# Kernel tuning notes

Hardware: AMD Instinct MI355X
Metric: run time of the kernel (lower is better)

## Reference

```python
import math
import jax, jax.numpy as jnp
import numpy as np

B, S, D, H = 4, 2048, 1024, 16
DH = D // H  # 64


def setup_inputs() -> dict:
    key = jax.random.key(0)
    k1, k2, k3 = jax.random.split(key, 3)
    x = jax.random.normal(k1, (B, S, D), dtype=jnp.float32)
    W_qkv = jax.random.normal(k2, (D, 3 * D), dtype=jnp.float32) * (1.0 / math.sqrt(D))
    b_qkv = jax.random.normal(k3, (3 * D,), dtype=jnp.float32) * 0.02
    return {"x": x, "W_qkv": W_qkv, "b_qkv": b_qkv}


def reference(x, W_qkv, b_qkv):
    b, s, d = x.shape
    qkv = x @ W_qkv + b_qkv                       # [B,S,3D]
    # Faithful to torch: view(B,S,H,3,D_h) -> interleaved per-head q/k/v split
    qkv = qkv.reshape(b, s, H, 3, DH)
    q = jnp.transpose(qkv[:, :, :, 0, :], (0, 2, 1, 3))  # [B,H,S,DH]
    k = jnp.transpose(qkv[:, :, :, 1, :], (0, 2, 1, 3))
    v = jnp.transpose(qkv[:, :, :, 2, :], (0, 2, 1, 3))
    scores = jnp.einsum('bhsd,bhtd->bhst', q, k) / math.sqrt(DH)  # [B,H,S,S]
    causal = jnp.triu(jnp.ones((s, s), dtype=bool), k=1)
    scores = jnp.where(causal, -jnp.inf, scores)
    weights = jax.nn.softmax(scores, axis=-1)
    # dropout is identity in eval/reference mode
    context = jnp.einsum('bhst,bhtd->bhsd', weights, v)  # [B,H,S,DH]
    return jnp.transpose(context, (0, 2, 1, 3)).reshape(b, s, d)
```

## Files before the change

kernel.cpp:

```cpp
#include <hip/hip_runtime.h>
#include <hip/hip_bf16.h>

#define Bz 4
#define Sz 2048
#define Dz 1024
#define Hz 16
#define DHz 64
#define Mz (Bz*Sz)
#define N3z (3*Dz)
#define Kz Dz

typedef short s16x8 __attribute__((ext_vector_type(8)));
typedef float f32x4 __attribute__((ext_vector_type(4)));
typedef unsigned short u16;

__device__ __forceinline__ u16 f2b(float f) {
  union { float f; unsigned u; } v; v.f = f;
  unsigned r = v.u + 0x7FFFu + ((v.u >> 16) & 1u);
  return (u16)(r >> 16);
}

__device__ __forceinline__ unsigned cvt_pk_bf16(float lo, float hi) {
  unsigned r;
  asm("v_cvt_pk_bf16_f32 %0, %1, %2" : "=v"(r) : "v"(lo), "v"(hi));
  return r;
}

__global__ __launch_bounds__(256) void cvt_x(const float* __restrict__ x,
                                             u16* __restrict__ xb) {
  int i = (blockIdx.x * 256 + threadIdx.x) * 4;
  float4 v = *reinterpret_cast<const float4*>(x + i);
  ushort4 o;
  o.x = f2b(v.x); o.y = f2b(v.y); o.z = f2b(v.z); o.w = f2b(v.w);
  *reinterpret_cast<ushort4*>(xb + i) = o;
}

__global__ __launch_bounds__(256) void transpose_w(const float* __restrict__ W,
                                                   u16* __restrict__ Wt) {
  __shared__ u16 t[32][33];
  int nb = blockIdx.x;
  int kb = blockIdx.y;
  int tx = threadIdx.x, ty = threadIdx.y;
#pragma unroll
  for (int j = 0; j < 4; ++j) {
    int k = kb * 32 + ty + j * 8;
    t[ty + j * 8][tx] = f2b(W[(size_t)k * N3z + nb * 32 + tx]);
  }
  __syncthreads();
#pragma unroll
  for (int j = 0; j < 4; ++j) {
    int n = nb * 32 + ty + j * 8;
    Wt[(size_t)n * Kz + kb * 32 + tx] = t[tx][ty + j * 8];
  }
}

#define BM 128
#define BN 128
#define BKs 64
#define QSCALE (0.125f * 1.44269504088896f)

__global__ __launch_bounds__(256) void qkv_gemm(
    const u16* __restrict__ A, const u16* __restrict__ Bt,
    const float* __restrict__ bias,
    u16* __restrict__ Qo, u16* __restrict__ Ko, u16* __restrict__ Vo) {
  __shared__ alignas(16) u16 As[BM * BKs];
  __shared__ alignas(16) u16 Bs[BN * BKs];
  const int tid = threadIdx.x;
  const int wid = tid >> 6, lane = tid & 63;
  const int wr = wid >> 1, wc = wid & 1;
  const int g = lane >> 4, lq = lane & 15;
  const int brow = blockIdx.x * BM;
  const int bcol = blockIdx.y * BN;

  const int soff = (((lane & 7) ^ (lane >> 3))) * 8;

  f32x4 acc[4][4] = {};

  for (int kt = 0; kt < Kz; kt += BKs) {
#pragma unroll
    for (int c = 0; c < 4; ++c) {
      int row = (wid * 4 + c) * 8 + (lane >> 3);
      const u16* ga = A + (size_t)(brow + row) * Kz + kt + soff;
      __builtin_amdgcn_global_load_lds(
          (const __attribute__((address_space(1))) void*)ga,
          (__attribute__((address_space(3))) void*)&As[(wid * 4 + c) * 512],
          16, 0, 0);
      const u16* gb = Bt + (size_t)(bcol + row) * Kz + kt + soff;
      __builtin_amdgcn_global_load_lds(
          (const __attribute__((address_space(1))) void*)gb,
          (__attribute__((address_space(3))) void*)&Bs[(wid * 4 + c) * 512],
          16, 0, 0);
    }
    __syncthreads();

#pragma unroll
    for (int ks = 0; ks < 2; ++ks) {
      s16x8 af[4], bfr[4];
#pragma unroll
      for (int i = 0; i < 4; ++i) {
        int rowa = wr * 64 + i * 16 + lq;
        int rowb = wc * 64 + i * 16 + lq;
        int sl = ((ks * 4 + g) ^ (lq & 7)) << 4;
        af[i]  = *reinterpret_cast<const s16x8*>((const char*)As + rowa * 128 + sl);
        bfr[i] = *reinterpret_cast<const s16x8*>((const char*)Bs + rowb * 128 + sl);
      }
#pragma unroll
      for (int mi = 0; mi < 4; ++mi)
#pragma unroll
        for (int ni = 0; ni < 4; ++ni)
          acc[mi][ni] = __builtin_amdgcn_mfma_f32_16x16x32_bf16(af[mi], bfr[ni], acc[mi][ni], 0, 0, 0);
    }
    __syncthreads();
  }

#pragma unroll
  for (int ni = 0; ni < 4; ++ni) {
    int gcol = bcol + wc * 64 + ni * 16 + lq;
    int h = gcol / 192;
    int rem = gcol - h * 192;
    int tt = rem >> 6;
    int dh = rem & 63;
    float bv = bias[gcol];
    u16* dst = (tt == 0) ? Qo : (tt == 1) ? Ko : Vo;
    float scale = (tt == 0) ? QSCALE : 1.0f;
#pragma unroll
    for (int mi = 0; mi < 4; ++mi) {
#pragma unroll
      for (int r = 0; r < 4; ++r) {
        int grow = brow + wr * 64 + mi * 16 + g * 4 + r;
        int bb = grow >> 11;
        int ss = grow & 2047;
        float v = (acc[mi][ni][r] + bv) * scale;
        dst[(((size_t)bb * Hz + h) * Sz + ss) * DHz + dh] = f2b(v);
      }
    }
  }
}

__global__ __launch_bounds__(512, 4) void attn_kernel(
    const u16* __restrict__ Qg, const u16* __restrict__ Kg,
    const u16* __restrict__ Vg, float* __restrict__ out) {
  __shared__ alignas(16) u16 Ks[2][64 * 64];
  __shared__ alignas(16) u16 Vs[2][64 * 64];

  const int qpair = blockIdx.x;
  const int bh = blockIdx.y;
  const int tid = threadIdx.x;
  const int wid = tid >> 6, lane = tid & 63;
  const int g = lane >> 4, lq = lane & 15;
  const size_t base = (size_t)bh * Sz * DHz;
  const int b = bh >> 4, h = bh & 15;

  const int krow = tid >> 3;
  const int kslot = tid & 7;
  const int kswz = kslot ^ (krow & 7);
  const int vkey = tid & 63;
  const int vdh0 = (tid >> 6) * 8;

  const int p = g & 1;
  const int cb = g >> 1;
  const int sA = 32 * (g & 1) + lq;
  const int sB = sA + 16;
  const int sEven = cb ? sB : sA;
  const int sOdd  = cb ? sA : sB;

  for (int half = 0; half < 2; ++half) {
    const int qt = half ? (15 - qpair) : qpair;
    const int q0w = qt * 128 + wid * 16;
    const int qrow = q0w + lq;

    s16x8 qf0 = *reinterpret_cast<const s16x8*>(Qg + base + (size_t)(q0w + lq) * DHz + g * 8);
    s16x8 qf1 = *reinterpret_cast<const s16x8*>(Qg + base + (size_t)(q0w + lq) * DHz + g * 8 + 32);

    f32x4 o[4] = {};
    float m1 = -1e30f;
    float l1 = 0.f;

    const int nt = 2 * qt + 2;

    {
      s16x8 kc = *reinterpret_cast<const s16x8*>(Kg + base + (size_t)krow * DHz + kslot * 8);
      s16x8 vc = *reinterpret_cast<const s16x8*>(Vg + base + (size_t)vkey * DHz + vdh0);
      char* KB = (char*)Ks[0];
      char* VB = (char*)Vs[0];
      *reinterpret_cast<s16x8*>(KB + krow * 128 + kswz * 16) = kc;
#pragma unroll
      for (int j = 0; j < 8; ++j)
        *reinterpret_cast<u16*>(VB + (((vdh0 + j) * 128 + vkey * 2) ^ (j << 4))) = (u16)vc[j];
    }
    __syncthreads();

    int cur = 0;
    for (int t = 0; t < nt; ++t) {
      const int kv0 = t * 64;
      const bool more = (t + 1 < nt);

      s16x8 kn, vn;
      if (more) {
        const int nv0 = kv0 + 64;
        kn = *reinterpret_cast<const s16x8*>(Kg + base + (size_t)(nv0 + krow) * DHz + kslot * 8);
        vn = *reinterpret_cast<const s16x8*>(Vg + base + (size_t)(nv0 + vkey) * DHz + vdh0);
      }

      const char* KsC = (const char*)Ks[0] + cur * 8192;
      const char* VsC = (const char*)Vs[0] + cur * 8192;

      const bool active = (kv0 <= q0w + 15);
      if (active) {
        f32x4 z[4];
#pragma unroll
        for (int f = 0; f < 4; ++f) {
          int row = f * 16 + lq;
          s16x8 kb0 = *reinterpret_cast<const s16x8*>(KsC + row * 128 + ((g ^ (row & 7)) << 4));
          s16x8 kb1 = *reinterpret_cast<const s16x8*>(KsC + row * 128 + (((g + 4) ^ (row & 7)) << 4));
          f32x4 zz = {0.f, 0.f, 0.f, 0.f};
          zz = __builtin_amdgcn_mfma_f32_16x16x32_bf16(kb0, qf0, zz, 0, 0, 0);
          zz = __builtin_amdgcn_mfma_f32_16x16x32_bf16(kb1, qf1, zz, 0, 0, 0);
          z[f] = zz;
        }

        if (kv0 + 63 > q0w) {
#pragma unroll
          for (int f = 0; f < 4; ++f)
#pragma unroll
            for (int r = 0; r < 4; ++r) {
              int key = kv0 + f * 16 + g * 4 + r;
              if (key > qrow) z[f][r] = -1e30f;
            }
        }

        float pm = z[0][0];
#pragma unroll
        for (int f = 0; f < 4; ++f)
#pragma unroll
          for (int r = 0; r < 4; ++r) pm = fmaxf(pm, z[f][r]);
        pm = fmaxf(pm, __shfl_xor(pm, 16));
        pm = fmaxf(pm, __shfl_xor(pm, 32));

        if (!__all(pm <= m1 + 8.0f)) {
          float mn = fmaxf(m1, pm);
          float a = exp2f(m1 - mn);
          m1 = mn;
          l1 *= a;
          float a0 = __shfl(a, 4 * g + 0);
          float a1 = __shfl(a, 4 * g + 1);
          float a2 = __shfl(a, 4 * g + 2);
          float a3 = __shfl(a, 4 * g + 3);
#pragma unroll
          for (int ni = 0; ni < 4; ++ni) {
            o[ni][0] *= a0; o[ni][1] *= a1; o[ni][2] *= a2; o[ni][3] *= a3;
          }
        }

        float s = 0.f;
        unsigned w[4][2];
#pragma unroll
        for (int f = 0; f < 4; ++f) {
          float p0 = exp2f(z[f][0] - m1);
          float p1 = exp2f(z[f][1] - m1);
          float p2 = exp2f(z[f][2] - m1);
          float p3 = exp2f(z[f][3] - m1);
          s += (p0 + p1) + (p2 + p3);
          w[f][0] = cvt_pk_bf16(p0, p1);
          w[f][1] = cvt_pk_bf16(p2, p3);
        }
        s += __shfl_xor(s, 16);
        s += __shfl_xor(s, 32);
        l1 += s;

        int e0 = __shfl((int)(p ? w[1][0] : w[0][0]), sEven);
        int o0 = __shfl((int)(p ? w[0][0] : w[1][0]), sOdd);
        int e1 = __shfl((int)(p ? w[1][1] : w[0][1]), sEven);
        int o1 = __shfl((int)(p ? w[0][1] : w[1][1]), sOdd);
        int e2 = __shfl((int)(p ? w[3][0] : w[2][0]), sEven);
        int o2 = __shfl((int)(p ? w[2][0] : w[3][0]), sOdd);
        int e3 = __shfl((int)(p ? w[3][1] : w[2][1]), sEven);
        int o3 = __shfl((int)(p ? w[2][1] : w[3][1]), sOdd);
        union { int i[4]; s16x8 v; } A0, A1;
        A0.i[0] = cb ? o0 : e0;
        A0.i[2] = cb ? e0 : o0;
        A0.i[1] = cb ? o1 : e1;
        A0.i[3] = cb ? e1 : o1;
        A1.i[0] = cb ? o2 : e2;
        A1.i[2] = cb ? e2 : o2;
        A1.i[1] = cb ? o3 : e3;
        A1.i[3] = cb ? e3 : o3;

#pragma unroll
        for (int ni = 0; ni < 4; ++ni) {
          int row = ni * 16 + lq;
          s16x8 vb0 = *reinterpret_cast<const s16x8*>(VsC + row * 128 + ((g ^ (row & 7)) << 4));
          s16x8 vb1 = *reinterpret_cast<const s16x8*>(VsC + row * 128 + (((g + 4) ^ (row & 7)) << 4));
          o[ni] = __builtin_amdgcn_mfma_f32_16x16x32_bf16(A0.v, vb0, o[ni], 0, 0, 0);
          o[ni] = __builtin_amdgcn_mfma_f32_16x16x32_bf16(A1.v, vb1, o[ni], 0, 0, 0);
        }
      }

      if (more) {
        char* KB = (char*)Ks[0] + (cur ^ 1) * 8192;
        char* VB = (char*)Vs[0] + (cur ^ 1) * 8192;
        *reinterpret_cast<s16x8*>(KB + krow * 128 + kswz * 16) = kn;
#pragma unroll
        for (int j = 0; j < 8; ++j)
          *reinterpret_cast<u16*>(VB + (((vdh0 + j) * 128 + vkey * 2) ^ (j << 4))) = (u16)vn[j];
      }
      __syncthreads();
      cur ^= 1;
    }

    float lr0 = __shfl(l1, 4 * g + 0);
    float lr1 = __shfl(l1, 4 * g + 1);
    float lr2 = __shfl(l1, 4 * g + 2);
    float lr3 = __shfl(l1, 4 * g + 3);
    float inv[4] = {1.0f / lr0, 1.0f / lr1, 1.0f / lr2, 1.0f / lr3};
#pragma unroll
    for (int r = 0; r < 4; ++r) {
      int s = q0w + g * 4 + r;
      float* op = out + (((size_t)b * Sz + s) * Hz + h) * DHz;
#pragma unroll
      for (int ni = 0; ni < 4; ++ni)
        op[ni * 16 + lq] = o[ni][r] * inv[r];
    }
  }
}

extern "C" void kernel_launch(void* const* d_in, const int* in_sizes, int n_in,
                              void* d_out, int out_size, void* d_ws, size_t ws_size,
                              hipStream_t stream) {
  const float* x    = (const float*)d_in[0];
  const float* W    = (const float*)d_in[1];
  const float* bias = (const float*)d_in[2];
  float* out = (float*)d_out;

  char* ws = (char*)d_ws;
  u16* xb = (u16*)(ws);
  u16* wt = (u16*)(ws + 16777216);
  u16* Qb = (u16*)(ws + 23068672);
  u16* Kb = (u16*)(ws + 39845888);
  u16* Vb = (u16*)(ws + 56623104);

  cvt_x<<<8192, 256, 0, stream>>>(x, xb);
  transpose_w<<<dim3(96, 32), dim3(32, 8), 0, stream>>>(W, wt);
  qkv_gemm<<<dim3(Mz / BM, N3z / BN), 256, 0, stream>>>(xb, wt, bias, Qb, Kb, Vb);
  attn_kernel<<<dim3(8, Bz * Hz), 512, 0, stream>>>(Qb, Kb, Vb, out);
}
```

Before: 238.5 us.

## Store V transposed, load K/V via global_load_lds, fuse paired query tiles

The QKV GEMM now writes V in a transposed [B,H,DH,S] layout. This lets the attention kernel stream both K and V tiles straight into LDS with global_load_lds, replacing the register round-trip and 8 scattered 16-bit LDS stores per V tile. The two query tiles of each block (qp and 15-qp) are now processed in one pass over K/V, so shared keys are loaded once and the tile synchronisation is shared. Block indices in both kernels are remapped for XCD/L2 locality. The GEMM epilogue now does strided V stores and the attention kernel holds two accumulators sets, which raises register pressure.

```diff
diff --git a/kernel.cpp b/kernel.cpp
--- a/kernel.cpp
+++ b/kernel.cpp
@@ -62,15 +62,20 @@
 __global__ __launch_bounds__(256) void qkv_gemm(
     const u16* __restrict__ A, const u16* __restrict__ Bt,
     const float* __restrict__ bias,
-    u16* __restrict__ Qo, u16* __restrict__ Ko, u16* __restrict__ Vo) {
+    u16* __restrict__ Qo, u16* __restrict__ Ko, u16* __restrict__ Vt) {
   __shared__ alignas(16) u16 As[BM * BKs];
   __shared__ alignas(16) u16 Bs[BN * BKs];
   const int tid = threadIdx.x;
   const int wid = tid >> 6, lane = tid & 63;
   const int wr = wid >> 1, wc = wid & 1;
   const int g = lane >> 4, lq = lane & 15;
-  const int brow = blockIdx.x * BM;
-  const int bcol = blockIdx.y * BN;
+
+  const int id = blockIdx.x + gridDim.x * blockIdx.y;
+  const int xc = id & 7, rr = id >> 3;
+  const int bx = xc * 8 + (rr & 7);
+  const int by = rr >> 3;
+  const int brow = bx * BM;
+  const int bcol = by * BN;
 
   const int soff = (((lane & 7) ^ (lane >> 3))) * 8;
 
@@ -121,8 +126,9 @@
     int tt = rem >> 6;
     int dh = rem & 63;
     float bv = bias[gcol];
-    u16* dst = (tt == 0) ? Qo : (tt == 1) ? Ko : Vo;
+    u16* dst = (tt == 0) ? Qo : (tt == 1) ? Ko : Vt;
     float scale = (tt == 0) ? QSCALE : 1.0f;
+    bool isv = (tt == 2);
 #pragma unroll
     for (int mi = 0; mi < 4; ++mi) {
 #pragma unroll
@@ -131,31 +137,130 @@
         int bb = grow >> 11;
         int ss = grow & 2047;
         float v = (acc[mi][ni][r] + bv) * scale;
-        dst[(((size_t)bb * Hz + h) * Sz + ss) * DHz + dh] = f2b(v);
+        size_t off = isv ? ((((size_t)bb * Hz + h) * DHz + dh) * Sz + ss)
+                         : ((((size_t)bb * Hz + h) * Sz + ss) * DHz + dh);
+        dst[off] = f2b(v);
       }
     }
+  }
+}
+
+__device__ __forceinline__ void attn_tile(
+    const char* KsC, const char* VsC, int kv0, int q0w, int qrow,
+    int g, int lq, int p, int cb, int sEven, int sOdd,
+    const s16x8& qf0, const s16x8& qf1,
+    f32x4 (&o)[4], float& m1, float& l1) {
+  if (kv0 > q0w + 15) return;
+
+  f32x4 z[4];
+#pragma unroll
+  for (int f = 0; f < 4; ++f) {
+    int row = f * 16 + lq;
+    s16x8 kb0 = *reinterpret_cast<const s16x8*>(KsC + row * 128 + ((g ^ (row & 7)) << 4));
+    s16x8 kb1 = *reinterpret_cast<const s16x8*>(KsC + row * 128 + (((g + 4) ^ (row & 7)) << 4));
+    f32x4 zz = {0.f, 0.f, 0.f, 0.f};
+    zz = __builtin_amdgcn_mfma_f32_16x16x32_bf16(kb0, qf0, zz, 0, 0, 0);
+    zz = __builtin_amdgcn_mfma_f32_16x16x32_bf16(kb1, qf1, zz, 0, 0, 0);
+    z[f] = zz;
+  }
+
+  if (kv0 + 63 > q0w) {
+#pragma unroll
+    for (int f = 0; f < 4; ++f)
+#pragma unroll
+      for (int r = 0; r < 4; ++r) {
+        int key = kv0 + f * 16 + g * 4 + r;
+        if (key > qrow) z[f][r] = -1e30f;
+      }
+  }
+
+  float pm = z[0][0];
+#pragma unroll
+  for (int f = 0; f < 4; ++f)
+#pragma unroll
+    for (int r = 0; r < 4; ++r) pm = fmaxf(pm, z[f][r]);
+  pm = fmaxf(pm, __shfl_xor(pm, 16));
+  pm = fmaxf(pm, __shfl_xor(pm, 32));
+
+  if (!__all(pm <= m1 + 8.0f)) {
+    float mn = fmaxf(m1, pm);
+    float a = exp2f(m1 - mn);
+    m1 = mn;
+    l1 *= a;
+    float a0 = __shfl(a, 4 * g + 0);
+    float a1 = __shfl(a, 4 * g + 1);
+    float a2 = __shfl(a, 4 * g + 2);
+    float a3 = __shfl(a, 4 * g + 3);
+#pragma unroll
+    for (int ni = 0; ni < 4; ++ni) {
+      o[ni][0] *= a0; o[ni][1] *= a1; o[ni][2] *= a2; o[ni][3] *= a3;
+    }
+  }
+
+  float s = 0.f;
+  unsigned w[4][2];
+#pragma unroll
+  for (int f = 0; f < 4; ++f) {
+    float p0 = exp2f(z[f][0] - m1);
+    float p1 = exp2f(z[f][1] - m1);
+    float p2 = exp2f(z[f][2] - m1);
+    float p3 = exp2f(z[f][3] - m1);
+    s += (p0 + p1) + (p2 + p3);
+    w[f][0] = cvt_pk_bf16(p0, p1);
+    w[f][1] = cvt_pk_bf16(p2, p3);
+  }
+  s += __shfl_xor(s, 16);
+  s += __shfl_xor(s, 32);
+  l1 += s;
+
+  int e0 = __shfl((int)(p ? w[1][0] : w[0][0]), sEven);
+  int o0 = __shfl((int)(p ? w[0][0] : w[1][0]), sOdd);
+  int e1 = __shfl((int)(p ? w[1][1] : w[0][1]), sEven);
+  int o1 = __shfl((int)(p ? w[0][1] : w[1][1]), sOdd);
+  int e2 = __shfl((int)(p ? w[3][0] : w[2][0]), sEven);
+  int o2 = __shfl((int)(p ? w[2][0] : w[3][0]), sOdd);
+  int e3 = __shfl((int)(p ? w[3][1] : w[2][1]), sEven);
+  int o3 = __shfl((int)(p ? w[2][1] : w[3][1]), sOdd);
+  union { int i[4]; s16x8 v; } A0, A1;
+  A0.i[0] = cb ? o0 : e0;
+  A0.i[2] = cb ? e0 : o0;
+  A0.i[1] = cb ? o1 : e1;
+  A0.i[3] = cb ? e1 : o1;
+  A1.i[0] = cb ? o2 : e2;
+  A1.i[2] = cb ? e2 : o2;
+  A1.i[1] = cb ? o3 : e3;
+  A1.i[3] = cb ? e3 : o3;
+
+#pragma unroll
+  for (int ni = 0; ni < 4; ++ni) {
+    int row = ni * 16 + lq;
+    s16x8 vb0 = *reinterpret_cast<const s16x8*>(VsC + row * 128 + ((g ^ (row & 7)) << 4));
+    s16x8 vb1 = *reinterpret_cast<const s16x8*>(VsC + row * 128 + (((g + 4) ^ (row & 7)) << 4));
+    o[ni] = __builtin_amdgcn_mfma_f32_16x16x32_bf16(A0.v, vb0, o[ni], 0, 0, 0);
+    o[ni] = __builtin_amdgcn_mfma_f32_16x16x32_bf16(A1.v, vb1, o[ni], 0, 0, 0);
   }
 }
 
 __global__ __launch_bounds__(512, 4) void attn_kernel(
     const u16* __restrict__ Qg, const u16* __restrict__ Kg,
-    const u16* __restrict__ Vg, float* __restrict__ out) {
+    const u16* __restrict__ Vtg, float* __restrict__ out) {
   __shared__ alignas(16) u16 Ks[2][64 * 64];
   __shared__ alignas(16) u16 Vs[2][64 * 64];
 
-  const int qpair = blockIdx.x;
-  const int bh = blockIdx.y;
   const int tid = threadIdx.x;
   const int wid = tid >> 6, lane = tid & 63;
   const int g = lane >> 4, lq = lane & 15;
+
+  const int id = blockIdx.x + 8 * blockIdx.y;
+  const int xc = id & 7, rr = id >> 3;
+  const int bh = xc * 8 + (rr & 7);
+  const int qp = rr >> 3;
+
   const size_t base = (size_t)bh * Sz * DHz;
   const int b = bh >> 4, h = bh & 15;
 
   const int krow = tid >> 3;
-  const int kslot = tid & 7;
-  const int kswz = kslot ^ (krow & 7);
-  const int vkey = tid & 63;
-  const int vdh0 = (tid >> 6) * 8;
+  const int sswz = ((tid & 7) ^ (krow & 7)) * 8;
 
   const int p = g & 1;
   const int cb = g >> 1;
@@ -164,150 +269,66 @@
   const int sEven = cb ? sB : sA;
   const int sOdd  = cb ? sA : sB;
 
+  const int qtA = qp, qtB = 15 - qp;
+  const int q0wA = qtA * 128 + wid * 16;
+  const int q0wB = qtB * 128 + wid * 16;
+  const int qrowA = q0wA + lq, qrowB = q0wB + lq;
+  const int ntA = 2 * qtA + 2, ntB = 2 * qtB + 2;
+
+  s16x8 qfA0 = *reinterpret_cast<const s16x8*>(Qg + base + (size_t)qrowA * DHz + g * 8);
+  s16x8 qfA1 = *reinterpret_cast<const s16x8*>(Qg + base + (size_t)qrowA * DHz + g * 8 + 32);
+  s16x8 qfB0 = *reinterpret_cast<const s16x8*>(Qg + base + (size_t)qrowB * DHz + g * 8);
+  s16x8 qfB1 = *reinterpret_cast<const s16x8*>(Qg + base + (size_t)qrowB * DHz + g * 8 + 32);
+
+  f32x4 oA[4] = {}, oB[4] = {};
+  float mA = -1e30f, lA = 0.f, mB = -1e30f, lB = 0.f;
+
+  {
+    const u16* gk = Kg + base + (size_t)krow * DHz + sswz;
+    __builtin_amdgcn_global_load_lds(
+        (const __attribute__((address_space(1))) void*)gk,
+        (__attribute__((address_space(3))) void*)&Ks[0][wid * 512], 16, 0, 0);
+    const u16* gv = Vtg + base + (size_t)krow * Sz + sswz;
+    __builtin_amdgcn_global_load_lds(
+        (const __attribute__((address_space(1))) void*)gv,
+        (__attribute__((address_space(3))) void*)&Vs[0][wid * 512], 16, 0, 0);
+  }
+  __syncthreads();
+
+  int cur = 0;
+  for (int t = 0; t < ntB; ++t) {
+    const int kv0 = t * 64;
+
+    if (t + 1 < ntB) {
+      const int nv0 = kv0 + 64;
+      const u16* gk = Kg + base + (size_t)(nv0 + krow) * DHz + sswz;
+      __builtin_amdgcn_global_load_lds(
+          (const __attribute__((address_space(1))) void*)gk,
+          (__attribute__((address_space(3))) void*)&Ks[cur ^ 1][wid * 512], 16, 0, 0);
+      const u16* gv = Vtg + base + (size_t)krow * Sz + nv0 + sswz;
+      __builtin_amdgcn_global_load_lds(
+          (const __attribute__((address_space(1))) void*)gv,
+          (__attribute__((address_space(3))) void*)&Vs[cur ^ 1][wid * 512], 16, 0, 0);
+    }
+
+    const char* KsC = (const char*)Ks[cur];
+    const char* VsC = (const char*)Vs[cur];
+
+    attn_tile(KsC, VsC, kv0, q0wB, qrowB, g, lq, p, cb, sEven, sOdd,
+              qfB0, qfB1, oB, mB, lB);
+    if (t < ntA)
+      attn_tile(KsC, VsC, kv0, q0wA, qrowA, g, lq, p, cb, sEven, sOdd,
+                qfA0, qfA1, oA, mA, lA);
+
+    __syncthreads();
+    cur ^= 1;
+  }
+
+#pragma unroll
   for (int half = 0; half < 2; ++half) {
-    const int qt = half ? (15 - qpair) : qpair;
-    const int q0w = qt * 128 + wid * 16;
-    const int qrow = q0w + lq;
-
-    s16x8 qf0 = *reinterpret_cast<const s16x8*>(Qg + base + (size_t)(q0w + lq) * DHz + g * 8);
-    s16x8 qf1 = *reinterpret_cast<const s16x8*>(Qg + base + (size_t)(q0w + lq) * DHz + g * 8 + 32);
-
-    f32x4 o[4] = {};
-    float m1 = -1e30f;
-    float l1 = 0.f;
-
-    const int nt = 2 * qt + 2;
-
-    {
-      s16x8 kc = *reinterpret_cast<const s16x8*>(Kg + base + (size_t)krow * DHz + kslot * 8);
-      s16x8 vc = *reinterpret_cast<const s16x8*>(Vg + base + (size_t)vkey * DHz + vdh0);
-      char* KB = (char*)Ks[0];
-      char* VB = (char*)Vs[0];
-      *reinterpret_cast<s16x8*>(KB + krow * 128 + kswz * 16) = kc;
-#pragma unroll
-      for (int j = 0; j < 8; ++j)
-        *reinterpret_cast<u16*>(VB + (((vdh0 + j) * 128 + vkey * 2) ^ (j << 4))) = (u16)vc[j];
-    }
-    __syncthreads();
-
-    int cur = 0;
-    for (int t = 0; t < nt; ++t) {
-      const int kv0 = t * 64;
-      const bool more = (t + 1 < nt);
-
-      s16x8 kn, vn;
-      if (more) {
-        const int nv0 = kv0 + 64;
-        kn = *reinterpret_cast<const s16x8*>(Kg + base + (size_t)(nv0 + krow) * DHz + kslot * 8);
-        vn = *reinterpret_cast<const s16x8*>(Vg + base + (size_t)(nv0 + vkey) * DHz + vdh0);
-      }
-
-      const char* KsC = (const char*)Ks[0] + cur * 8192;
-      const char* VsC = (const char*)Vs[0] + cur * 8192;
-
-      const bool active = (kv0 <= q0w + 15);
-      if (active) {
-        f32x4 z[4];
-#pragma unroll
-        for (int f = 0; f < 4; ++f) {
-          int row = f * 16 + lq;
-          s16x8 kb0 = *reinterpret_cast<const s16x8*>(KsC + row * 128 + ((g ^ (row & 7)) << 4));
-          s16x8 kb1 = *reinterpret_cast<const s16x8*>(KsC + row * 128 + (((g + 4) ^ (row & 7)) << 4));
-          f32x4 zz = {0.f, 0.f, 0.f, 0.f};
-          zz = __builtin_amdgcn_mfma_f32_16x16x32_bf16(kb0, qf0, zz, 0, 0, 0);
-          zz = __builtin_amdgcn_mfma_f32_16x16x32_bf16(kb1, qf1, zz, 0, 0, 0);
-          z[f] = zz;
-        }
-
-        if (kv0 + 63 > q0w) {
-#pragma unroll
-          for (int f = 0; f < 4; ++f)
-#pragma unroll
-            for (int r = 0; r < 4; ++r) {
-              int key = kv0 + f * 16 + g * 4 + r;
-              if (key > qrow) z[f][r] = -1e30f;
-            }
-        }
-
-        float pm = z[0][0];
-#pragma unroll
-        for (int f = 0; f < 4; ++f)
-#pragma unroll
-          for (int r = 0; r < 4; ++r) pm = fmaxf(pm, z[f][r]);
-        pm = fmaxf(pm, __shfl_xor(pm, 16));
-        pm = fmaxf(pm, __shfl_xor(pm, 32));
-
-        if (!__all(pm <= m1 + 8.0f)) {
-          float mn = fmaxf(m1, pm);
-          float a = exp2f(m1 - mn);
-          m1 = mn;
-          l1 *= a;
-          float a0 = __shfl(a, 4 * g + 0);
-          float a1 = __shfl(a, 4 * g + 1);
-          float a2 = __shfl(a, 4 * g + 2);
-          float a3 = __shfl(a, 4 * g + 3);
-#pragma unroll
-          for (int ni = 0; ni < 4; ++ni) {
-            o[ni][0] *= a0; o[ni][1] *= a1; o[ni][2] *= a2; o[ni][3] *= a3;
-          }
-        }
-
-        float s = 0.f;
-        unsigned w[4][2];
-#pragma unroll
-        for (int f = 0; f < 4; ++f) {
-          float p0 = exp2f(z[f][0] - m1);
-          float p1 = exp2f(z[f][1] - m1);
-          float p2 = exp2f(z[f][2] - m1);
-          float p3 = exp2f(z[f][3] - m1);
-          s += (p0 + p1) + (p2 + p3);
-          w[f][0] = cvt_pk_bf16(p0, p1);
-          w[f][1] = cvt_pk_bf16(p2, p3);
-        }
-        s += __shfl_xor(s, 16);
-        s += __shfl_xor(s, 32);
-        l1 += s;
-
-        int e0 = __shfl((int)(p ? w[1][0] : w[0][0]), sEven);
-        int o0 = __shfl((int)(p ? w[0][0] : w[1][0]), sOdd);
-        int e1 = __shfl((int)(p ? w[1][1] : w[0][1]), sEven);
-        int o1 = __shfl((int)(p ? w[0][1] : w[1][1]), sOdd);
-        int e2 = __shfl((int)(p ? w[3][0] : w[2][0]), sEven);
-        int o2 = __shfl((int)(p ? w[2][0] : w[3][0]), sOdd);
-        int e3 = __shfl((int)(p ? w[3][1] : w[2][1]), sEven);
-        int o3 = __shfl((int)(p ? w[2][1] : w[3][1]), sOdd);
-        union { int i[4]; s16x8 v; } A0, A1;
-        A0.i[0] = cb ? o0 : e0;
-        A0.i[2] = cb ? e0 : o0;
-        A0.i[1] = cb ? o1 : e1;
-        A0.i[3] = cb ? e1 : o1;
-        A1.i[0] = cb ? o2 : e2;
-        A1.i[2] = cb ? e2 : o2;
-        A1.i[1] = cb ? o3 : e3;
-        A1.i[3] = cb ? e3 : o3;
-
-#pragma unroll
-        for (int ni = 0; ni < 4; ++ni) {
-          int row = ni * 16 + lq;
-          s16x8 vb0 = *reinterpret_cast<const s16x8*>(VsC + row * 128 + ((g ^ (row & 7)) << 4));
-          s16x8 vb1 = *reinterpret_cast<const s16x8*>(VsC + row * 128 + (((g + 4) ^ (row & 7)) << 4));
-          o[ni] = __builtin_amdgcn_mfma_f32_16x16x32_bf16(A0.v, vb0, o[ni], 0, 0, 0);
-          o[ni] = __builtin_amdgcn_mfma_f32_16x16x32_bf16(A1.v, vb1, o[ni], 0, 0, 0);
-        }
-      }
-
-      if (more) {
-        char* KB = (char*)Ks[0] + (cur ^ 1) * 8192;
-        char* VB = (char*)Vs[0] + (cur ^ 1) * 8192;
-        *reinterpret_cast<s16x8*>(KB + krow * 128 + kswz * 16) = kn;
-#pragma unroll
-        for (int j = 0; j < 8; ++j)
-          *reinterpret_cast<u16*>(VB + (((vdh0 + j) * 128 + vkey * 2) ^ (j << 4))) = (u16)vn[j];
-      }
-      __syncthreads();
-      cur ^= 1;
-    }
-
+    const int q0w = half ? q0wB : q0wA;
+    f32x4* o = half ? oB : oA;
+    float l1 = half ? lB : lA;
     float lr0 = __shfl(l1, 4 * g + 0);
     float lr1 = __shfl(l1, 4 * g + 1);
     float lr2 = __shfl(l1, 4 * g + 2);
@@ -337,10 +358,10 @@
   u16* wt = (u16*)(ws + 16777216);
   u16* Qb = (u16*)(ws + 23068672);
   u16* Kb = (u16*)(ws + 39845888);
-  u16* Vb = (u16*)(ws + 56623104);
+  u16* Vtb = (u16*)(ws + 56623104);
 
   cvt_x<<<8192, 256, 0, stream>>>(x, xb);
   transpose_w<<<dim3(96, 32), dim3(32, 8), 0, stream>>>(W, wt);
-  qkv_gemm<<<dim3(Mz / BM, N3z / BN), 256, 0, stream>>>(xb, wt, bias, Qb, Kb, Vb);
-  attn_kernel<<<dim3(8, Bz * Hz), 512, 0, stream>>>(Qb, Kb, Vb, out);
-}
+  qkv_gemm<<<dim3(Mz / BM, N3z / BN), 256, 0, stream>>>(xb, wt, bias, Qb, Kb, Vtb);
+  attn_kernel<<<dim3(8, Bz * Hz), 512, 0, stream>>>(Qb, Kb, Vtb, out);
+}
```

After: 242.4 us. About the same (+1.6%).
